# Optimization experiments

Measured on AMD Instinct MI355X. Metric: run time of the kernel, lower is better.

Reference implementation:

```python
import jax, jax.numpy as jnp
import numpy as np

B, T, C = 128, 256, 384   # batch, seq (== BLOCK_SIZE), embed dim
H, D = 6, 64              # heads, head_dim
M = 128                   # memory prefix length
WIN = 64                  # local window


def setup_inputs() -> dict:
    key = jax.random.key(0)
    ks = jax.random.split(key, 6)
    s = 0.02
    return {
        "x": jax.random.normal(ks[0], (B, T, C), jnp.float32),
        "memory": jax.random.normal(ks[1], (M, C), jnp.float32),
        "W_qkv": (jax.random.normal(ks[2], (C, 3 * C), jnp.float32) * s),
        "b_qkv": jnp.zeros((3 * C,), jnp.float32),
        "W_proj": (jax.random.normal(ks[3], (C, C), jnp.float32) * s),
        "b_proj": jnp.zeros((C,), jnp.float32),
        "gate": jnp.ones((C,), jnp.float32),
    }


def reference(x, memory, W_qkv, b_qkv, W_proj, b_proj, gate):
    Bx, Tx, Cx = x.shape
    Mx = memory.shape[0]
    Tt = Tx + Mx

    qkv = x @ W_qkv + b_qkv                      # [B,T,3C]
    q, k, v = jnp.split(qkv, 3, axis=-1)
    mem = jnp.broadcast_to(memory[None], (Bx, Mx, Cx))
    k = jnp.concatenate([mem, k], axis=1)        # [B,Tt,C]
    v = jnp.concatenate([mem, v], axis=1)

    qh = q.reshape(Bx, Tx, H, D)
    kh = k.reshape(Bx, Tt, H, D)
    vh = v.reshape(Bx, Tt, H, D)

    att = jnp.einsum('bqhd,bkhd->bhqk', qh, kh) * (1.0 / jnp.sqrt(jnp.float32(D)))

    # self part (last T columns): causal AND local window; memory prefix unmasked
    i = jnp.arange(Tx)[:, None]
    j = jnp.arange(Tx)[None, :]
    self_mask = (j <= i) & (jnp.abs(i - j) <= WIN)            # [T,T]
    full_mask = jnp.concatenate(
        [jnp.ones((Tx, Mx), bool), self_mask], axis=1)        # [T,Tt]
    att = jnp.where(full_mask[None, None], att, -jnp.inf)
    att = jax.nn.softmax(att, axis=-1)

    y = jnp.einsum('bhqk,bkhd->bqhd', att, vh).reshape(Bx, Tx, Cx)
    return (y * gate) @ W_proj + b_proj
```

## Files before the change

### kernel.cpp

```cpp
#include <hip/hip_runtime.h>

#define B_   128
#define T_   256
#define C_   384
#define H_   6
#define D_   64
#define M_   128
#define WIN_ 64
#define C3_  1152
#define QKS_ 768

typedef unsigned int   uint;
typedef unsigned short ushort;
typedef __attribute__((ext_vector_type(8))) short bf16x8;
typedef __attribute__((ext_vector_type(4))) float f32x4;

#define AS1 __attribute__((address_space(1)))
#define AS3 __attribute__((address_space(3)))
#define MFMA16(a,b,c) __builtin_amdgcn_mfma_f32_16x16x32_bf16((a),(b),(c),0,0,0)
#define SCHED_FENCE() __builtin_amdgcn_sched_barrier(0)

__device__ __forceinline__ ushort f2bf(float f) {
  union { float f; uint u; } c; c.f = f;
  uint x = c.u;
  return (ushort)((x + 0x7fffu + ((x >> 16) & 1u)) >> 16);
}
__device__ __forceinline__ uint cvtpk(float lo, float hi) {
  uint r;
  asm("v_cvt_pk_bf16_f32 %0, %1, %2" : "=v"(r) : "v"(lo), "v"(hi));
  return r;
}
__device__ __forceinline__ void gload_lds16(const ushort* g, ushort* l) {
  __builtin_amdgcn_global_load_lds((const AS1 uint*)g, (AS3 uint*)l, 16, 0, 0);
}

#define NX4_  ((B_ * T_ * C_) / 4)
#define NM4_  ((M_ * C_) / 4)
#define NMT_  (H_ * 64 * 128)
#define NWQ_  (C_ * C3_)
#define NWP_  (C_ * C_)

__global__ __launch_bounds__(256)
void k_prep(const float* __restrict__ x, const float* __restrict__ memory,
            const float* __restrict__ Wq, const float* __restrict__ Wp,
            ushort* __restrict__ x_bf, ushort* __restrict__ mem_bf,
            ushort* __restrict__ memT, ushort* __restrict__ Wq_t,
            ushort* __restrict__ Wp_t)
{
  int id = blockIdx.x * 256 + threadIdx.x;
  if (id < NX4_) {
    float4 f = ((const float4*)x)[id];
    ushort4 u; u.x = f2bf(f.x); u.y = f2bf(f.y); u.z = f2bf(f.z); u.w = f2bf(f.w);
    *(ushort4*)&x_bf[id * 4] = u;
    return;
  }
  id -= NX4_;
  if (id < NM4_) {
    float4 f = ((const float4*)memory)[id];
    ushort4 u; u.x = f2bf(f.x); u.y = f2bf(f.y); u.z = f2bf(f.z); u.w = f2bf(f.w);
    *(ushort4*)&mem_bf[id * 4] = u;
    return;
  }
  id -= NM4_;
  if (id < NMT_) {
    int k = id & 127;
    int hd = id >> 7;
    int h = hd >> 6, d = hd & 63;
    memT[id] = f2bf(memory[(size_t)k * C_ + h * 64 + d]);
    return;
  }
  id -= NMT_;
  if (id < NWQ_) {
    int n = id / C_, k = id % C_;
    Wq_t[id] = f2bf(Wq[(size_t)k * C3_ + n]);
    return;
  }
  id -= NWQ_;
  if (id < NWP_) {
    int n = id / C_, k = id % C_;
    Wp_t[id] = f2bf(Wp[(size_t)k * C_ + n]);
  }
}

__global__ __launch_bounds__(512, 4)
void k_gemm0(const ushort* __restrict__ A, const ushort* __restrict__ Bt,
             const float* __restrict__ bias, ushort* __restrict__ qkw,
             ushort* __restrict__ vTw)
{
  __shared__ __align__(16) ushort smem[36864];
  constexpr int NT = 9;
  const int wg = blockIdx.x;
  const int X = wg & 7, j = wg >> 3;
  const int bmT = X * 16 + j / NT;
  const int by = j - (j / NT) * NT;
  const int bm = bmT * 256, bn = by * 128;
  const int tid = threadIdx.x;
  const int lane = tid & 63, w = tid >> 6;
  const int wr = w >> 1, wc = w & 1;
  const int g = lane >> 4, l15 = lane & 15;

  f32x4 acc[4][4] = {};

  auto stage = [&](int buf, int k0) {
    #pragma unroll
    for (int i = 0; i < 2; ++i) {
      int s = i * 512 + tid;
      int row = s >> 2, cS = s & 3;
      int c = cS ^ ((row >> 1) & 3);
      gload_lds16(A + (size_t)(bm + row) * C_ + k0 + c * 8, &smem[buf * 8192 + s * 8]);
    }
    {
      int s = tid;
      int row = s >> 2, cS = s & 3;
      int c = cS ^ ((row >> 1) & 3);
      gload_lds16(Bt + (size_t)(bn + row) * C_ + k0 + c * 8, &smem[24576 + buf * 4096 + s * 8]);
    }
  };

  stage(0, 0);
  stage(1, 32);
  SCHED_FENCE();
  asm volatile("s_waitcnt vmcnt(3)" ::: "memory");
  __builtin_amdgcn_s_barrier();
  SCHED_FENCE();

  #pragma unroll
  for (int t = 0; t < 12; ++t) {
    const int cur = t % 3;
    if (t < 10) stage((t + 2) % 3, (t + 2) * 32);

    bf16x8 af[4], bfr[4];
    #pragma unroll
    for (int m = 0; m < 4; ++m) {
      int row = wr * 64 + m * 16 + l15;
      int c = g ^ ((row >> 1) & 3);
      af[m] = *(const bf16x8*)&smem[cur * 8192 + row * 32 + c * 8];
    }
    #pragma unroll
    for (int n = 0; n < 4; ++n) {
      int row = wc * 64 + n * 16 + l15;
      int c = g ^ ((row >> 1) & 3);
      bfr[n] = *(const bf16x8*)&smem[24576 + cur * 4096 + row * 32 + c * 8];
    }
    #pragma unroll
    for (int m = 0; m < 4; ++m)
      #pragma unroll
      for (int n = 0; n < 4; ++n)
        acc[m][n] = MFMA16(af[m], bfr[n], acc[m][n]);

    if (t < 11) {
      SCHED_FENCE();
      if (t < 10) asm volatile("s_waitcnt vmcnt(3)" ::: "memory");
      else        asm volatile("s_waitcnt vmcnt(0)" ::: "memory");
      __builtin_amdgcn_s_barrier();
      SCHED_FENCE();
    }
  }

  if (by < 6) {
    __syncthreads();
    #pragma unroll
    for (int m = 0; m < 4; ++m)
      #pragma unroll
      for (int n = 0; n < 4; ++n) {
        int colL = wc * 64 + n * 16 + l15;
        float bv = bias[bn + colL];
        #pragma unroll
        for (int r = 0; r < 4; ++r) {
          int rowL = wr * 64 + m * 16 + g * 4 + r;
          smem[rowL * 128 + (colL ^ ((rowL & 7) << 3))] = f2bf(acc[m][n][r] + bv);
        }
      }
    __syncthreads();
    #pragma unroll
    for (int i = 0; i < 8; ++i) {
      int rowL = (tid >> 2) + (i >> 2) * 128;
      int slot = (i & 3) * 4 + (tid & 3);
      int c = slot * 8;
      bf16x8 vv = *(const bf16x8*)&smem[rowL * 128 + (c ^ ((rowL & 7) << 3))];
      *(bf16x8*)(qkw + (size_t)(bm + rowL) * QKS_ + bn + c) = vv;
    }
  } else {
    ushort (*CsT)[272] = (ushort(*)[272])smem;
    __syncthreads();
    #pragma unroll
    for (int m = 0; m < 4; ++m)
      #pragma unroll
      for (int n = 0; n < 4; ++n) {
        int colL = wc * 64 + n * 16 + l15;
        float bv = bias[bn + colL];
        int row0 = wr * 64 + m * 16 + g * 4;
        uint lo = (uint)f2bf(acc[m][n][0] + bv) | ((uint)f2bf(acc[m][n][1] + bv) << 16);
        uint hi = (uint)f2bf(acc[m][n][2] + bv) | ((uint)f2bf(acc[m][n][3] + bv) << 16);
        uint2 uu; uu.x = lo; uu.y = hi;
        *(uint2*)&CsT[colL][row0] = uu;
      }
    __syncthreads();
    #pragma unroll
    for (int i = 0; i < 8; ++i) {
      int s = i * 512 + tid;
      int colL = s >> 5;
      int kc = s & 31;
      int ch = (bn - 768) + colL;
      int hh = ch >> 6, dd = ch & 63;
      bf16x8 vv = *(const bf16x8*)&CsT[colL][kc * 8];
      *(bf16x8*)(vTw + ((size_t)(bmT * H_ + hh) * 64 + dd) * 256 + kc * 8) = vv;
    }
  }
}

__global__ __launch_bounds__(256, 3)
void k_gemm1(const ushort* __restrict__ A, const ushort* __restrict__ Bt,
             const float* __restrict__ bias, float* __restrict__ outf)
{
  __shared__ __align__(16) ushort smem[24576];
  constexpr int NT = 3;
  const int wg = blockIdx.x;
  const int X = wg & 7, j = wg >> 3;
  const int bmT = X * 32 + j / NT;
  const int by = j - (j / NT) * NT;
  const int bm = bmT * 128, bn = by * 128;
  const int tid = threadIdx.x;
  const int lane = tid & 63, w = tid >> 6;
  const int wr = w >> 1, wc = w & 1;
  const int g = lane >> 4, l15 = lane & 15;

  f32x4 acc[4][4] = {};

  auto stage = [&](int buf, int k0) {
    #pragma unroll
    for (int i = 0; i < 2; ++i) {
      int s = i * 256 + tid;
      int row = s >> 2, cS = s & 3;
      int c = cS ^ ((row >> 1) & 3);
      gload_lds16(A  + (size_t)(bm + row) * C_ + k0 + c * 8, &smem[buf * 4096 + s * 8]);
      gload_lds16(Bt + (size_t)(bn + row) * C_ + k0 + c * 8, &smem[12288 + buf * 4096 + s * 8]);
    }
  };

  stage(0, 0);
  stage(1, 32);
  SCHED_FENCE();
  asm volatile("s_waitcnt vmcnt(4)" ::: "memory");
  __builtin_amdgcn_s_barrier();
  SCHED_FENCE();

  #pragma unroll
  for (int t = 0; t < 12; ++t) {
    const int cur = t % 3;
    if (t < 10) stage((t + 2) % 3, (t + 2) * 32);

    bf16x8 af[4], bfr[4];
    #pragma unroll
    for (int m = 0; m < 4; ++m) {
      int row = wr * 64 + m * 16 + l15;
      int c = g ^ ((row >> 1) & 3);
      af[m] = *(const bf16x8*)&smem[cur * 4096 + row * 32 + c * 8];
    }
    #pragma unroll
    for (int n = 0; n < 4; ++n) {
      int row = wc * 64 + n * 16 + l15;
      int c = g ^ ((row >> 1) & 3);
      bfr[n] = *(const bf16x8*)&smem[12288 + cur * 4096 + row * 32 + c * 8];
    }
    #pragma unroll
    for (int m = 0; m < 4; ++m)
      #pragma unroll
      for (int n = 0; n < 4; ++n)
        acc[m][n] = MFMA16(af[m], bfr[n], acc[m][n]);

    if (t < 11) {
      SCHED_FENCE();
      if (t < 10) asm volatile("s_waitcnt vmcnt(4)" ::: "memory");
      else        asm volatile("s_waitcnt vmcnt(0)" ::: "memory");
      __builtin_amdgcn_s_barrier();
      SCHED_FENCE();
    }
  }

  #pragma unroll
  for (int m = 0; m < 4; ++m)
    #pragma unroll
    for (int n = 0; n < 4; ++n) {
      int col = bn + wc * 64 + n * 16 + l15;
      float bv = bias[col];
      #pragma unroll
      for (int r = 0; r < 4; ++r) {
        int row = bm + wr * 64 + m * 16 + g * 4 + r;
        outf[(size_t)row * C_ + col] = acc[m][n][r] + bv;
      }
    }
}

__global__ __launch_bounds__(512, 4)
void k_attn(const ushort* __restrict__ qkw, const ushort* __restrict__ vTw,
            const ushort* __restrict__ membf, const ushort* __restrict__ memT,
            const float* __restrict__ gate, ushort* __restrict__ y)
{
  __shared__ ushort Ks[2][384][32];
  __shared__ ushort Pb[8][32 * 32];

  const int b = blockIdx.x, h = blockIdx.y;
  const int tid = threadIdx.x, lane = tid & 63, w = tid >> 6;
  const int g = lane >> 4, l15 = lane & 15;
  const int q0 = w * 32;

  const ushort* qbase = qkw + (size_t)b * T_ * QKS_ + h * 64;
  const ushort* kcols = qbase + C_;
  const ushort* vbase = vTw + (size_t)(b * H_ + h) * 64 * 256;
  const ushort* mTb   = memT + (size_t)h * 64 * 128;
  const ushort* mKb   = membf + h * 64;

  #pragma unroll
  for (int i = 0; i < 6; ++i) {
    int s = i * 512 + tid;
    int kk = s / 1536, r4 = s - kk * 1536;
    int row = r4 >> 2, cS = r4 & 3;
    int c = cS ^ ((row >> 1) & 3);
    const ushort* src = (row < M_)
        ? mKb + (size_t)row * C_ + kk * 32 + c * 8
        : kcols + (size_t)(row - M_) * QKS_ + kk * 32 + c * 8;
    gload_lds16(src, &Ks[0][0][0] + s * 8);
  }

  bf16x8 qf[2][2];
  #pragma unroll
  for (int m = 0; m < 2; ++m)
    #pragma unroll
    for (int kk = 0; kk < 2; ++kk)
      qf[m][kk] = *(const bf16x8*)(qbase + (size_t)(q0 + m * 16 + l15) * QKS_ + kk * 32 + g * 8);

  __syncthreads();

  f32x4 yacc[2][4] = {};
  float rsum[2][4] = {};
  ushort* P = &Pb[w][0];

  const int c0 = (q0 >= WIN_) ? ((q0 - WIN_) >> 5) : 0;
  const int nch_self = (q0 >> 5) - c0 + 1;
  const int ss = M_ + c0 * 32;

  for (int ch = 0; ch < 4 + nch_self; ++ch) {
    const bool is_mem = (ch < 4);
    const int r0 = is_mem ? ch * 32 : ss + (ch - 4) * 32;
    const ushort* vsrc = is_mem ? mTb : vbase;
    const int vld = is_mem ? 128 : 256;
    const int keyoff = is_mem ? r0 : (r0 - M_);

    f32x4 s_[2][2];
    #pragma unroll
    for (int m = 0; m < 2; ++m)
      #pragma unroll
      for (int n = 0; n < 2; ++n)
        s_[m][n] = (f32x4){0.f, 0.f, 0.f, 0.f};
    __builtin_amdgcn_s_setprio(1);
    #pragma unroll
    for (int n = 0; n < 2; ++n) {
      int R = r0 + n * 16 + l15;
      int c = g ^ ((R >> 1) & 3);
      #pragma unroll
      for (int kk = 0; kk < 2; ++kk) {
        bf16x8 kf = *(const bf16x8*)&Ks[kk][R][c * 8];
        #pragma unroll
        for (int m = 0; m < 2; ++m)
          s_[m][n] = MFMA16(qf[m][kk], kf, s_[m][n]);
      }
    }
    __builtin_amdgcn_s_setprio(0);

    bf16x8 vb[4];
    #pragma unroll
    for (int n = 0; n < 4; ++n) {
      int dd = n * 16 + l15;
      vb[n] = *(const bf16x8*)(vsrc + (size_t)dd * vld + keyoff + g * 8);
    }

    #pragma unroll
    for (int m = 0; m < 2; ++m)
      #pragma unroll
      for (int n = 0; n < 2; ++n) {
        int key_row = r0 + n * 16 + l15;
        int jj = key_row - M_;
        int kc = n * 16 + l15;
        float p[4];
        #pragma unroll
        for (int r = 0; r < 4; ++r) {
          int qi = q0 + m * 16 + g * 4 + r;
          bool ok = is_mem || ((jj <= qi) && (qi - jj <= WIN_));
          float e = ok ? exp2f(s_[m][n][r] * 0.18033688011112042f) : 0.f;
          rsum[m][r] += e;
          p[r] = e;
        }
        uint u01 = cvtpk(p[0], p[1]);
        uint u23 = cvtpk(p[2], p[3]);
        #pragma unroll
        for (int r = 0; r < 4; ++r) {
          int ql = m * 16 + g * 4 + r;
          int sig = ((ql >> 1) ^ (ql >> 2)) & 3;
          uint u = (r < 2) ? u01 : u23;
          ushort val = (r & 1) ? (ushort)(u >> 16) : (ushort)(u & 0xffffu);
          P[ql * 32 + (kc ^ (sig << 3))] = val;
        }
      }

    bf16x8 pa[2];
    #pragma unroll
    for (int m = 0; m < 2; ++m) {
      int row = m * 16 + l15;
      int sig = ((row >> 1) ^ (row >> 2)) & 3;
      pa[m] = *(const bf16x8*)&P[row * 32 + ((g ^ sig) << 3)];
    }
    __builtin_amdgcn_s_setprio(1);
    #pragma unroll
    for (int n = 0; n < 4; ++n)
      #pragma unroll
      for (int m = 0; m < 2; ++m)
        yacc[m][n] = MFMA16(pa[m], vb[n], yacc[m][n]);
    __builtin_amdgcn_s_setprio(0);
  }

  float inv[2][4];
  #pragma unroll
  for (int m = 0; m < 2; ++m)
    #pragma unroll
    for (int r = 0; r < 4; ++r) {
      float v = rsum[m][r];
      v += __shfl_xor(v, 1); v += __shfl_xor(v, 2);
      v += __shfl_xor(v, 4); v += __shfl_xor(v, 8);
      inv[m][r] = 1.f / v;
    }

  #pragma unroll
  for (int m = 0; m < 2; ++m)
    #pragma unroll
    for (int n = 0; n < 4; ++n) {
      int dd = n * 16 + l15;
      float gv = gate[h * 64 + dd];
      #pragma unroll
      for (int r = 0; r < 4; ++r) {
        int qi = q0 + m * 16 + g * 4 + r;
        y[(size_t)(b * T_ + qi) * C_ + h * 64 + dd] = f2bf(yacc[m][n][r] * inv[m][r] * gv);
      }
    }
}

extern "C" void kernel_launch(void* const* d_in, const int* in_sizes, int n_in,
                              void* d_out, int out_size, void* d_ws, size_t ws_size,
                              hipStream_t stream) {
  const float* x      = (const float*)d_in[0];
  const float* memory = (const float*)d_in[1];
  const float* W_qkv  = (const float*)d_in[2];
  const float* b_qkv  = (const float*)d_in[3];
  const float* W_proj = (const float*)d_in[4];
  const float* b_proj = (const float*)d_in[5];
  const float* gate   = (const float*)d_in[6];
  float* out = (float*)d_out;

  ushort* p = (ushort*)d_ws;
  ushort* Wq_t  = p;  p += (size_t)C_ * C3_;
  ushort* Wp_t  = p;  p += (size_t)C_ * C_;
  ushort* membf = p;  p += (size_t)M_ * C_;
  ushort* memT  = p;  p += (size_t)NMT_;
  ushort* qkw   = p;  p += (size_t)B_ * T_ * QKS_;
  ushort* vTw   = p;  p += (size_t)B_ * T_ * C_;
  ushort* xybf  = p;  p += (size_t)B_ * T_ * C_;

  dim3 blk(256);

  int prep_items = NX4_ + NM4_ + NMT_ + NWQ_ + NWP_;
  k_prep<<<dim3((prep_items + 255) / 256), blk, 0, stream>>>(
      x, memory, W_qkv, W_proj, xybf, membf, memT, Wq_t, Wp_t);

  k_gemm0<<<dim3(1152), dim3(512), 0, stream>>>(xybf, Wq_t, b_qkv, qkw, vTw);

  k_attn<<<dim3(B_, H_), dim3(512), 0, stream>>>(qkw, vTw, membf, memT, gate, xybf);

  k_gemm1<<<dim3(768), blk, 0, stream>>>(xybf, Wp_t, b_proj, out);
}
```

Baseline: 109.3 us.

## Shrink QKV GEMM LDS to double buffering and two-pass epilogue for occupancy

Cuts the QKV GEMM kernel's shared memory from 72KB to 48KB by going from a 3-stage to a 2-stage load pipeline. The epilogue is split into two passes over 128-row halves so the output staging fits the smaller buffer. Launch bounds rise to 6 blocks per CU to get more resident workgroups for latency hiding. In exchange, each iteration now waits for all outstanding loads (vmcnt(0)), which weakens overlap of global loads with MFMA, and the epilogue gains extra barriers.

```diff
diff --git a/kernel.cpp b/kernel.cpp
--- a/kernel.cpp
+++ b/kernel.cpp
@@ -82,12 +82,12 @@
   }
 }
 
-__global__ __launch_bounds__(512, 4)
+__global__ __launch_bounds__(512, 6)
 void k_gemm0(const ushort* __restrict__ A, const ushort* __restrict__ Bt,
              const float* __restrict__ bias, ushort* __restrict__ qkw,
              ushort* __restrict__ vTw)
 {
-  __shared__ __align__(16) ushort smem[36864];
+  __shared__ __align__(16) ushort smem[24576];
   constexpr int NT = 9;
   const int wg = blockIdx.x;
   const int X = wg & 7, j = wg >> 3;
@@ -113,21 +113,20 @@
       int s = tid;
       int row = s >> 2, cS = s & 3;
       int c = cS ^ ((row >> 1) & 3);
-      gload_lds16(Bt + (size_t)(bn + row) * C_ + k0 + c * 8, &smem[24576 + buf * 4096 + s * 8]);
+      gload_lds16(Bt + (size_t)(bn + row) * C_ + k0 + c * 8, &smem[16384 + buf * 4096 + s * 8]);
     }
   };
 
   stage(0, 0);
-  stage(1, 32);
   SCHED_FENCE();
-  asm volatile("s_waitcnt vmcnt(3)" ::: "memory");
+  asm volatile("s_waitcnt vmcnt(0)" ::: "memory");
   __builtin_amdgcn_s_barrier();
   SCHED_FENCE();
 
   #pragma unroll
   for (int t = 0; t < 12; ++t) {
-    const int cur = t % 3;
-    if (t < 10) stage((t + 2) % 3, (t + 2) * 32);
+    const int cur = t & 1;
+    if (t < 11) stage(cur ^ 1, (t + 1) * 32);
 
     bf16x8 af[4], bfr[4];
     #pragma unroll
@@ -140,7 +139,7 @@
     for (int n = 0; n < 4; ++n) {
       int row = wc * 64 + n * 16 + l15;
       int c = g ^ ((row >> 1) & 3);
-      bfr[n] = *(const bf16x8*)&smem[24576 + cur * 4096 + row * 32 + c * 8];
+      bfr[n] = *(const bf16x8*)&smem[16384 + cur * 4096 + row * 32 + c * 8];
     }
     #pragma unroll
     for (int m = 0; m < 4; ++m)
@@ -150,61 +149,72 @@
 
     if (t < 11) {
       SCHED_FENCE();
-      if (t < 10) asm volatile("s_waitcnt vmcnt(3)" ::: "memory");
-      else        asm volatile("s_waitcnt vmcnt(0)" ::: "memory");
+      asm volatile("s_waitcnt vmcnt(0)" ::: "memory");
       __builtin_amdgcn_s_barrier();
       SCHED_FENCE();
     }
   }
 
   if (by < 6) {
-    __syncthreads();
-    #pragma unroll
-    for (int m = 0; m < 4; ++m)
-      #pragma unroll
-      for (int n = 0; n < 4; ++n) {
-        int colL = wc * 64 + n * 16 + l15;
-        float bv = bias[bn + colL];
+    #pragma unroll
+    for (int p = 0; p < 2; ++p) {
+      __syncthreads();
+      if (wr >> 1 == p) {
         #pragma unroll
-        for (int r = 0; r < 4; ++r) {
-          int rowL = wr * 64 + m * 16 + g * 4 + r;
-          smem[rowL * 128 + (colL ^ ((rowL & 7) << 3))] = f2bf(acc[m][n][r] + bv);
-        }
-      }
-    __syncthreads();
-    #pragma unroll
-    for (int i = 0; i < 8; ++i) {
-      int rowL = (tid >> 2) + (i >> 2) * 128;
-      int slot = (i & 3) * 4 + (tid & 3);
-      int c = slot * 8;
-      bf16x8 vv = *(const bf16x8*)&smem[rowL * 128 + (c ^ ((rowL & 7) << 3))];
-      *(bf16x8*)(qkw + (size_t)(bm + rowL) * QKS_ + bn + c) = vv;
+        for (int m = 0; m < 4; ++m)
+          #pragma unroll
+          for (int n = 0; n < 4; ++n) {
+            int colL = wc * 64 + n * 16 + l15;
+            float bv = bias[bn + colL];
+            #pragma unroll
+            for (int r = 0; r < 4; ++r) {
+              int rowL = wr * 64 + m * 16 + g * 4 + r;
+              int rowL2 = rowL - p * 128;
+              smem[rowL2 * 128 + (colL ^ ((rowL2 & 7) << 3))] = f2bf(acc[m][n][r] + bv);
+            }
+          }
+      }
+      __syncthreads();
+      #pragma unroll
+      for (int i = 0; i < 4; ++i) {
+        int s = i * 512 + tid;
+        int rowL2 = s >> 4;
+        int slot = s & 15;
+        int c = slot * 8;
+        bf16x8 vv = *(const bf16x8*)&smem[rowL2 * 128 + (c ^ ((rowL2 & 7) << 3))];
+        *(bf16x8*)(qkw + (size_t)(bm + p * 128 + rowL2) * QKS_ + bn + c) = vv;
+      }
     }
   } else {
-    ushort (*CsT)[272] = (ushort(*)[272])smem;
-    __syncthreads();
-    #pragma unroll
-    for (int m = 0; m < 4; ++m)
-      #pragma unroll
-      for (int n = 0; n < 4; ++n) {
-        int colL = wc * 64 + n * 16 + l15;
-        float bv = bias[bn + colL];
-        int row0 = wr * 64 + m * 16 + g * 4;
-        uint lo = (uint)f2bf(acc[m][n][0] + bv) | ((uint)f2bf(acc[m][n][1] + bv) << 16);
-        uint hi = (uint)f2bf(acc[m][n][2] + bv) | ((uint)f2bf(acc[m][n][3] + bv) << 16);
-        uint2 uu; uu.x = lo; uu.y = hi;
-        *(uint2*)&CsT[colL][row0] = uu;
-      }
-    __syncthreads();
-    #pragma unroll
-    for (int i = 0; i < 8; ++i) {
-      int s = i * 512 + tid;
-      int colL = s >> 5;
-      int kc = s & 31;
-      int ch = (bn - 768) + colL;
-      int hh = ch >> 6, dd = ch & 63;
-      bf16x8 vv = *(const bf16x8*)&CsT[colL][kc * 8];
-      *(bf16x8*)(vTw + ((size_t)(bmT * H_ + hh) * 64 + dd) * 256 + kc * 8) = vv;
+    ushort (*CsT)[136] = (ushort(*)[136])smem;
+    #pragma unroll
+    for (int p = 0; p < 2; ++p) {
+      __syncthreads();
+      if (wr >> 1 == p) {
+        #pragma unroll
+        for (int m = 0; m < 4; ++m)
+          #pragma unroll
+          for (int n = 0; n < 4; ++n) {
+            int colL = wc * 64 + n * 16 + l15;
+            float bv = bias[bn + colL];
+            int row0 = wr * 64 + m * 16 + g * 4 - p * 128;
+            uint lo = (uint)f2bf(acc[m][n][0] + bv) | ((uint)f2bf(acc[m][n][1] + bv) << 16);
+            uint hi = (uint)f2bf(acc[m][n][2] + bv) | ((uint)f2bf(acc[m][n][3] + bv) << 16);
+            uint2 uu; uu.x = lo; uu.y = hi;
+            *(uint2*)&CsT[colL][row0] = uu;
+          }
+      }
+      __syncthreads();
+      #pragma unroll
+      for (int i = 0; i < 4; ++i) {
+        int s = i * 512 + tid;
+        int colL = s >> 4;
+        int kc = s & 15;
+        int ch = (bn - 768) + colL;
+        int hh = ch >> 6, dd = ch & 63;
+        bf16x8 vv = *(const bf16x8*)&CsT[colL][kc * 8];
+        *(bf16x8*)(vTw + ((size_t)(bmT * H_ + hh) * 64 + dd) * 256 + p * 128 + kc * 8) = vv;
+      }
     }
   }
 }
```

After: 246.4 us. 2.25x slower.
